# Kernel optimization log

Measured on AMD Instinct MI355X. Metric: run time of the kernel, lower is better.

The kernel has to match this reference:

```python
import jax, jax.numpy as jnp
import numpy as np

BATCH, SEQ, D_MODEL, K_SIZE = 2, 4096, 2048, 3


def setup_inputs() -> dict:
    key = jax.random.key(0)
    k1, k2, k3, k4 = jax.random.split(key, 4)
    s = 1.0 / np.sqrt(D_MODEL)
    x = jax.random.normal(k1, (BATCH, SEQ, D_MODEL), dtype=jnp.float32)
    w1 = jax.random.normal(k2, (3 * D_MODEL, D_MODEL), dtype=jnp.float32) * s
    w2 = jax.random.normal(k3, (D_MODEL, D_MODEL), dtype=jnp.float32) * s
    conv_w = jax.random.normal(k4, (D_MODEL, 1, K_SIZE), dtype=jnp.float32) * 0.5
    return {"x": x, "w1": w1, "w2": w2, "conv_w": conv_w}


def _causal_depthwise_conv(u, conv_w):
    # u: [B, D, S]; conv_w: [D, 1, K] (torch Conv1d weight layout, groups=D)
    k = conv_w.shape[-1]
    return jax.lax.conv_general_dilated(
        u, conv_w,
        window_strides=(1,),
        padding=[(k - 1, 0)],  # left pad = causal; matches pad=k-1 then [..., :seq_len]
        feature_group_count=u.shape[1],
        dimension_numbers=("NCH", "OIH", "NCH"),
    )


def reference(x, w1, w2, conv_w):
    # x: [B, S, D]
    BCx = jnp.einsum("bsd,ed->bse", x, w1)           # [B, S, 3D]
    Bg, Cg, Xg = jnp.split(BCx, 3, axis=-1)           # each [B, S, D]
    u = (Bg * Xg).transpose(0, 2, 1)                  # [B, D, S]
    conv_out = _causal_depthwise_conv(u, conv_w)      # [B, D, S]
    gated = Cg * conv_out.transpose(0, 2, 1)          # [B, S, D]
    return jnp.einsum("bsd,ed->bse", gated, w2)       # [B, S, D]
```

## Files before the change

kernel.cpp:

```cpp
#include <hip/hip_runtime.h>
#include <stdint.h>

#define BATCH 2
#define SEQ   4096
#define DM    2048
#define MT    (BATCH*SEQ)
#define N1    (3*DM)
#define STRIP 16

typedef __attribute__((ext_vector_type(8))) __bf16 bf16x8;
typedef __attribute__((ext_vector_type(4))) float  f32x4;
typedef __attribute__((ext_vector_type(8))) unsigned short ushort8v;
typedef __attribute__((ext_vector_type(4))) unsigned short ushort4v;

__device__ inline unsigned short f2bf(float f) {
    uint32_t u = __float_as_uint(f);
    u += 0x7FFFu + ((u >> 16) & 1u);
    return (unsigned short)(u >> 16);
}
__device__ inline float bf2f(unsigned short h) {
    return __uint_as_float(((uint32_t)h) << 16);
}

__global__ void cvt_f32_bf16(const float* __restrict__ src,
                             unsigned short* __restrict__ dst, int n) {
    int i = (blockIdx.x * blockDim.x + threadIdx.x) * 4;
    const int stride = gridDim.x * blockDim.x * 4;
    for (; i < n; i += stride) {
        const float4 v = *(const float4*)(src + i);
        ushort4v o;
        o[0] = f2bf(v.x); o[1] = f2bf(v.y); o[2] = f2bf(v.z); o[3] = f2bf(v.w);
        *(ushort4v*)(dst + i) = o;
    }
}

__device__ inline void async_copy16(const void* g, void* l) {
    __builtin_amdgcn_global_load_lds(
        (const __attribute__((address_space(1))) void*)g,
        (__attribute__((address_space(3))) void*)l,
        16, 0, 0);
}


#define MFMA_(d, a, b) d = __builtin_amdgcn_mfma_f32_16x16x32_bf16(a, b, d, 0, 0, 0)

#define QUAD(MH, NH, BQ) do { \
  MFMA_(acc[(MH)*4+0][(NH)*2+0], af[0][0], BQ[0][0]); MFMA_(acc[(MH)*4+0][(NH)*2+0], af[0][1], BQ[0][1]); \
  MFMA_(acc[(MH)*4+0][(NH)*2+1], af[0][0], BQ[1][0]); MFMA_(acc[(MH)*4+0][(NH)*2+1], af[0][1], BQ[1][1]); \
  MFMA_(acc[(MH)*4+1][(NH)*2+0], af[1][0], BQ[0][0]); MFMA_(acc[(MH)*4+1][(NH)*2+0], af[1][1], BQ[0][1]); \
  MFMA_(acc[(MH)*4+1][(NH)*2+1], af[1][0], BQ[1][0]); MFMA_(acc[(MH)*4+1][(NH)*2+1], af[1][1], BQ[1][1]); \
  MFMA_(acc[(MH)*4+2][(NH)*2+0], af[2][0], BQ[0][0]); MFMA_(acc[(MH)*4+2][(NH)*2+0], af[2][1], BQ[0][1]); \
  MFMA_(acc[(MH)*4+2][(NH)*2+1], af[2][0], BQ[1][0]); MFMA_(acc[(MH)*4+2][(NH)*2+1], af[2][1], BQ[1][1]); \
  MFMA_(acc[(MH)*4+3][(NH)*2+0], af[3][0], BQ[0][0]); MFMA_(acc[(MH)*4+3][(NH)*2+0], af[3][1], BQ[0][1]); \
  MFMA_(acc[(MH)*4+3][(NH)*2+1], af[3][0], BQ[1][0]); MFMA_(acc[(MH)*4+3][(NH)*2+1], af[3][1], BQ[1][1]); \
} while (0)

template <bool OUT_BF16>
__global__ __launch_bounds__(512)
void gemm256(const unsigned short* __restrict__ A,
             const unsigned short* __restrict__ B,
             void* __restrict__ Cout, int M, int N, int K) {
    __shared__ __attribute__((aligned(16))) char lds[131072];
    const int tid  = threadIdx.x;
    const int wave = tid >> 6;
    const int lane = tid & 63;
    const int wr = wave >> 2, wc = wave & 3;
    const int l16 = lane & 15, lh = lane >> 4;
    const int NT = K >> 6;

    const int nx = gridDim.x;
    int flat = blockIdx.y * nx + blockIdx.x;
    const int cpx = (nx * gridDim.y) >> 3;
    flat = (flat & 7) * cpx + (flat >> 3);
    const int blockN = (flat % nx) << 8;
    const int blockM = (flat / nx) << 8;

    const int swze = ((((lane & 7) << 4) ^ ((lane >> 3) << 4)) >> 1);
    const int sr   = (wave << 3) + (lane >> 3);
    const unsigned short* Ab = A + (size_t)blockM * K;
    const unsigned short* Bb = B + (size_t)blockN * K;
    const size_t a00 = (size_t)(sr      ) * K + swze;
    const size_t a01 = (size_t)(sr +  64) * K + swze;
    const size_t a10 = (size_t)(sr + 128) * K + swze;
    const size_t a11 = (size_t)(sr + 192) * K + swze;
    const int bsr = ((wave >> 2) << 6) + ((wave & 3) << 3) + (lane >> 3);
    const size_t b00 = (size_t)(bsr      ) * K + swze;
    const size_t b01 = (size_t)(bsr + 128) * K + swze;
    const size_t b10 = (size_t)(bsr +  32) * K + swze;
    const size_t b11 = (size_t)(bsr + 160) * K + swze;
    const int ldsw = wave << 10;

#define STG_A(BUF, U, K0) do { \
    async_copy16(Ab + a##U##0 + (K0), lds + (BUF) + (U)*16384 + ldsw); \
    async_copy16(Ab + a##U##1 + (K0), lds + (BUF) + (U)*16384 + 8192 + ldsw); } while (0)
#define STG_B(BUF, NH, K0) do { \
    async_copy16(Bb + b##NH##0 + (K0), lds + (BUF) + 32768 + (NH)*16384 + ldsw); \
    async_copy16(Bb + b##NH##1 + (K0), lds + (BUF) + 32768 + (NH)*16384 + 8192 + ldsw); } while (0)

    const int rdswz = (l16 & 7) << 4;
    const int ac0 = ((lh << 4)      ) ^ rdswz;
    const int ac1 = (64 + (lh << 4)) ^ rdswz;
    const int aRB = wr * 16384 + l16 * 128;
    const int bRB = 32768 + (wc * 32 + l16) * 128;

#define LDA_(BUF, I, C) (*(const bf16x8*)(lds + (BUF) + aRB + (I)*2048 + (C)))
#define LDB_(BUF, J, C) (*(const bf16x8*)(lds + (BUF) + bRB + ((J)>>1)*16384 + ((J)&1)*2048 + (C)))

    f32x4 acc[8][4] = {};
    bf16x8 af[4][2], bq0[2][2], bq1[2][2];

    STG_B(0, 0, 0); STG_B(0, 1, 0); STG_A(0, 0, 0); STG_A(0, 1, 0);
    if (NT > 1) {
        STG_B(65536, 0, 64); STG_B(65536, 1, 64); STG_A(65536, 0, 64);
        asm volatile("s_waitcnt vmcnt(6)" ::: "memory");
    } else {
        asm volatile("s_waitcnt vmcnt(0)" ::: "memory");
    }
    __builtin_amdgcn_s_barrier();

#define ITER(CUR, NXT, T) do { \
     \
    af[0][0]=LDA_(CUR,0,ac0); af[0][1]=LDA_(CUR,0,ac1); \
    af[1][0]=LDA_(CUR,1,ac0); af[1][1]=LDA_(CUR,1,ac1); \
    af[2][0]=LDA_(CUR,2,ac0); af[2][1]=LDA_(CUR,2,ac1); \
    af[3][0]=LDA_(CUR,3,ac0); af[3][1]=LDA_(CUR,3,ac1); \
    bq0[0][0]=LDB_(CUR,0,ac0); bq0[0][1]=LDB_(CUR,0,ac1); \
    bq0[1][0]=LDB_(CUR,1,ac0); bq0[1][1]=LDB_(CUR,1,ac1); \
    if ((T) + 1 < NT) STG_A(NXT, 1, ((T)+1)*64); \
    __builtin_amdgcn_s_barrier(); \
    asm volatile("s_waitcnt lgkmcnt(0)" ::: "memory"); \
    __builtin_amdgcn_s_setprio(1); \
    QUAD(0, 0, bq0); \
    __builtin_amdgcn_s_setprio(0); \
    __builtin_amdgcn_s_barrier(); \
     \
    bq1[0][0]=LDB_(CUR,2,ac0); bq1[0][1]=LDB_(CUR,2,ac1); \
    bq1[1][0]=LDB_(CUR,3,ac0); bq1[1][1]=LDB_(CUR,3,ac1); \
    if ((T) + 2 < NT) STG_B(CUR, 0, ((T)+2)*64); \
    __builtin_amdgcn_s_barrier(); \
    asm volatile("s_waitcnt lgkmcnt(0)" ::: "memory"); \
    __builtin_amdgcn_s_setprio(1); \
    QUAD(0, 1, bq1); \
    __builtin_amdgcn_s_setprio(0); \
    __builtin_amdgcn_s_barrier(); \
     \
    af[0][0]=LDA_(CUR,4,ac0); af[0][1]=LDA_(CUR,4,ac1); \
    af[1][0]=LDA_(CUR,5,ac0); af[1][1]=LDA_(CUR,5,ac1); \
    af[2][0]=LDA_(CUR,6,ac0); af[2][1]=LDA_(CUR,6,ac1); \
    af[3][0]=LDA_(CUR,7,ac0); af[3][1]=LDA_(CUR,7,ac1); \
    if ((T) + 2 < NT) STG_B(CUR, 1, ((T)+2)*64); \
    __builtin_amdgcn_s_barrier(); \
    asm volatile("s_waitcnt lgkmcnt(0)" ::: "memory"); \
    __builtin_amdgcn_s_setprio(1); \
    QUAD(1, 1, bq1); \
    __builtin_amdgcn_s_setprio(0); \
    __builtin_amdgcn_s_barrier(); \
     \
    if ((T) + 2 < NT) STG_A(CUR, 0, ((T)+2)*64); \
    __builtin_amdgcn_s_barrier(); \
    __builtin_amdgcn_s_setprio(1); \
    QUAD(1, 0, bq0); \
    __builtin_amdgcn_s_setprio(0); \
    if ((T) + 2 < NT)      { asm volatile("s_waitcnt vmcnt(6)" ::: "memory"); } \
    else if ((T) + 1 < NT) { asm volatile("s_waitcnt vmcnt(0)" ::: "memory"); } \
    __builtin_amdgcn_s_barrier(); \
} while (0)

    for (int t = 0; t < NT; t += 2) {
        ITER(0, 65536, t);
        ITER(65536, 0, t + 1);
    }

    const int orow = blockM + wr * 128 + (lh << 2);
    const int ocol = blockN + wc * 64 + l16;
    #pragma unroll
    for (int i = 0; i < 8; ++i) {
        #pragma unroll
        for (int j = 0; j < 4; ++j) {
            #pragma unroll
            for (int r = 0; r < 4; ++r) {
                const int row = orow + i * 16 + r;
                const int col = ocol + j * 16;
                if constexpr (OUT_BF16)
                    ((unsigned short*)Cout)[(size_t)row * N + col] = f2bf(acc[i][j][r]);
                else
                    ((float*)Cout)[(size_t)row * N + col] = acc[i][j][r];
            }
        }
    }
#undef ITER
#undef LDA_
#undef LDB_
#undef STG_A
#undef STG_B
}

__global__ void conv_gate_kernel(const unsigned short* __restrict__ BCx,
                                 const float* __restrict__ cw,
                                 unsigned short* __restrict__ gated) {
    const int tid = threadIdx.x;
    const int d0  = tid * 8;
    const int nstrips = SEQ / STRIP;
    const int b   = blockIdx.x / nstrips;
    const int s0  = (blockIdx.x % nstrips) * STRIP;

    float w0[8], w1c[8], w2c[8];
    #pragma unroll
    for (int c = 0; c < 8; ++c) {
        w0[c]  = cw[(d0 + c) * 3 + 0];
        w1c[c] = cw[(d0 + c) * 3 + 1];
        w2c[c] = cw[(d0 + c) * 3 + 2];
    }

    float um1[8], um2[8];
    if (s0 > 0) {
        const unsigned short* r2 = BCx + (size_t)(b * SEQ + s0 - 2) * N1;
        const unsigned short* r1 = BCx + (size_t)(b * SEQ + s0 - 1) * N1;
        ushort8v bg2 = *(const ushort8v*)(r2 + d0);
        ushort8v xg2 = *(const ushort8v*)(r2 + 2 * DM + d0);
        ushort8v bg1 = *(const ushort8v*)(r1 + d0);
        ushort8v xg1 = *(const ushort8v*)(r1 + 2 * DM + d0);
        #pragma unroll
        for (int c = 0; c < 8; ++c) {
            um2[c] = bf2f(bg2[c]) * bf2f(xg2[c]);
            um1[c] = bf2f(bg1[c]) * bf2f(xg1[c]);
        }
    } else {
        #pragma unroll
        for (int c = 0; c < 8; ++c) { um2[c] = 0.f; um1[c] = 0.f; }
    }

    for (int s = s0; s < s0 + STRIP; ++s) {
        const size_t m = (size_t)b * SEQ + s;
        const unsigned short* rp = BCx + m * N1;
        ushort8v bg = *(const ushort8v*)(rp + d0);
        ushort8v cg = *(const ushort8v*)(rp + DM + d0);
        ushort8v xg = *(const ushort8v*)(rp + 2 * DM + d0);
        ushort8v og;
        #pragma unroll
        for (int c = 0; c < 8; ++c) {
            const float u    = bf2f(bg[c]) * bf2f(xg[c]);
            const float conv = w0[c] * um2[c] + w1c[c] * um1[c] + w2c[c] * u;
            const float g    = bf2f(cg[c]) * conv;
            um2[c] = um1[c];
            um1[c] = u;
            og[c]  = f2bf(g);
        }
        *(ushort8v*)(gated + m * DM + d0) = og;
    }
}

extern "C" void kernel_launch(void* const* d_in, const int* in_sizes, int n_in,
                              void* d_out, int out_size, void* d_ws, size_t ws_size,
                              hipStream_t stream) {
    const float* x   = (const float*)d_in[0];
    const float* w1  = (const float*)d_in[1];
    const float* w2  = (const float*)d_in[2];
    const float* cw  = (const float*)d_in[3];
    float* out = (float*)d_out;

    char* ws = (char*)d_ws;
    unsigned short* x_bf   = (unsigned short*)ws;
    unsigned short* w1_bf  = x_bf  + (size_t)MT * DM;
    unsigned short* w2_bf  = w1_bf + (size_t)N1 * DM;
    unsigned short* bcx_bf = w2_bf + (size_t)DM * DM;
    unsigned short* g_bf   = bcx_bf + (size_t)MT * N1;

    cvt_f32_bf16<<<2048, 256, 0, stream>>>(x,  x_bf,  MT * DM);
    cvt_f32_bf16<<<1024, 256, 0, stream>>>(w1, w1_bf, N1 * DM);
    cvt_f32_bf16<<<512,  256, 0, stream>>>(w2, w2_bf, DM * DM);

    gemm256<true><<<dim3(N1 / 256, MT / 256), 512, 0, stream>>>(
        x_bf, w1_bf, bcx_bf, MT, N1, DM);

    conv_gate_kernel<<<BATCH * (SEQ / STRIP), 256, 0, stream>>>(bcx_bf, cw, g_bf);

    gemm256<false><<<dim3(DM / 256, MT / 256), 512, 0, stream>>>(
        g_bf, w2_bf, out, MT, DM, DM);
}
```

Measured before the change: 311.7 us.

## Double-buffer A fragments and prefetch next tile's fragments across iterations

Splits the A register fragments into low and high halves so both stay live, reorders the four MFMA quadrants so each LDS read is issued one phase ahead with partial lgkmcnt waits, and preloads the next K-tile's first fragments at the end of each iteration. It also restructures the global-to-LDS staging schedule, prefetching the whole second tile up front and adjusting the vmcnt thresholds. The aim is to hide LDS read latency behind MFMA work and cut the full lgkmcnt(0) stalls, at the cost of more VGPRs and a more fragile barrier and waitcnt ordering.

```diff
diff --git a/kernel.cpp b/kernel.cpp
--- a/kernel.cpp
+++ b/kernel.cpp
@@ -44,15 +44,15 @@
 
 #define MFMA_(d, a, b) d = __builtin_amdgcn_mfma_f32_16x16x32_bf16(a, b, d, 0, 0, 0)
 
-#define QUAD(MH, NH, BQ) do { \
-  MFMA_(acc[(MH)*4+0][(NH)*2+0], af[0][0], BQ[0][0]); MFMA_(acc[(MH)*4+0][(NH)*2+0], af[0][1], BQ[0][1]); \
-  MFMA_(acc[(MH)*4+0][(NH)*2+1], af[0][0], BQ[1][0]); MFMA_(acc[(MH)*4+0][(NH)*2+1], af[0][1], BQ[1][1]); \
-  MFMA_(acc[(MH)*4+1][(NH)*2+0], af[1][0], BQ[0][0]); MFMA_(acc[(MH)*4+1][(NH)*2+0], af[1][1], BQ[0][1]); \
-  MFMA_(acc[(MH)*4+1][(NH)*2+1], af[1][0], BQ[1][0]); MFMA_(acc[(MH)*4+1][(NH)*2+1], af[1][1], BQ[1][1]); \
-  MFMA_(acc[(MH)*4+2][(NH)*2+0], af[2][0], BQ[0][0]); MFMA_(acc[(MH)*4+2][(NH)*2+0], af[2][1], BQ[0][1]); \
-  MFMA_(acc[(MH)*4+2][(NH)*2+1], af[2][0], BQ[1][0]); MFMA_(acc[(MH)*4+2][(NH)*2+1], af[2][1], BQ[1][1]); \
-  MFMA_(acc[(MH)*4+3][(NH)*2+0], af[3][0], BQ[0][0]); MFMA_(acc[(MH)*4+3][(NH)*2+0], af[3][1], BQ[0][1]); \
-  MFMA_(acc[(MH)*4+3][(NH)*2+1], af[3][0], BQ[1][0]); MFMA_(acc[(MH)*4+3][(NH)*2+1], af[3][1], BQ[1][1]); \
+#define QUAD(MH, NH, AF, BQ) do { \
+  MFMA_(acc[(MH)*4+0][(NH)*2+0], AF[0][0], BQ[0][0]); MFMA_(acc[(MH)*4+0][(NH)*2+0], AF[0][1], BQ[0][1]); \
+  MFMA_(acc[(MH)*4+0][(NH)*2+1], AF[0][0], BQ[1][0]); MFMA_(acc[(MH)*4+0][(NH)*2+1], AF[0][1], BQ[1][1]); \
+  MFMA_(acc[(MH)*4+1][(NH)*2+0], AF[1][0], BQ[0][0]); MFMA_(acc[(MH)*4+1][(NH)*2+0], AF[1][1], BQ[0][1]); \
+  MFMA_(acc[(MH)*4+1][(NH)*2+1], AF[1][0], BQ[1][0]); MFMA_(acc[(MH)*4+1][(NH)*2+1], AF[1][1], BQ[1][1]); \
+  MFMA_(acc[(MH)*4+2][(NH)*2+0], AF[2][0], BQ[0][0]); MFMA_(acc[(MH)*4+2][(NH)*2+0], AF[2][1], BQ[0][1]); \
+  MFMA_(acc[(MH)*4+2][(NH)*2+1], AF[2][0], BQ[1][0]); MFMA_(acc[(MH)*4+2][(NH)*2+1], AF[2][1], BQ[1][1]); \
+  MFMA_(acc[(MH)*4+3][(NH)*2+0], AF[3][0], BQ[0][0]); MFMA_(acc[(MH)*4+3][(NH)*2+0], AF[3][1], BQ[0][1]); \
+  MFMA_(acc[(MH)*4+3][(NH)*2+1], AF[3][0], BQ[1][0]); MFMA_(acc[(MH)*4+3][(NH)*2+1], AF[3][1], BQ[1][1]); \
 } while (0)
 
 template <bool OUT_BF16>
@@ -107,30 +107,34 @@
 #define LDB_(BUF, J, C) (*(const bf16x8*)(lds + (BUF) + bRB + ((J)>>1)*16384 + ((J)&1)*2048 + (C)))
 
     f32x4 acc[8][4] = {};
-    bf16x8 af[4][2], bq0[2][2], bq1[2][2];
+    bf16x8 afL[4][2], afH[4][2], bq0[2][2], bq1[2][2];
 
     STG_B(0, 0, 0); STG_B(0, 1, 0); STG_A(0, 0, 0); STG_A(0, 1, 0);
     if (NT > 1) {
-        STG_B(65536, 0, 64); STG_B(65536, 1, 64); STG_A(65536, 0, 64);
-        asm volatile("s_waitcnt vmcnt(6)" ::: "memory");
+        STG_B(65536, 0, 64); STG_B(65536, 1, 64);
+        STG_A(65536, 0, 64); STG_A(65536, 1, 64);
+        asm volatile("s_waitcnt vmcnt(8)" ::: "memory");
     } else {
         asm volatile("s_waitcnt vmcnt(0)" ::: "memory");
     }
     __builtin_amdgcn_s_barrier();
+    afL[0][0]=LDA_(0,0,ac0); afL[0][1]=LDA_(0,0,ac1);
+    afL[1][0]=LDA_(0,1,ac0); afL[1][1]=LDA_(0,1,ac1);
+    afL[2][0]=LDA_(0,2,ac0); afL[2][1]=LDA_(0,2,ac1);
+    afL[3][0]=LDA_(0,3,ac0); afL[3][1]=LDA_(0,3,ac1);
+    bq0[0][0]=LDB_(0,0,ac0); bq0[0][1]=LDB_(0,0,ac1);
+    bq0[1][0]=LDB_(0,1,ac0); bq0[1][1]=LDB_(0,1,ac1);
 
 #define ITER(CUR, NXT, T) do { \
      \
-    af[0][0]=LDA_(CUR,0,ac0); af[0][1]=LDA_(CUR,0,ac1); \
-    af[1][0]=LDA_(CUR,1,ac0); af[1][1]=LDA_(CUR,1,ac1); \
-    af[2][0]=LDA_(CUR,2,ac0); af[2][1]=LDA_(CUR,2,ac1); \
-    af[3][0]=LDA_(CUR,3,ac0); af[3][1]=LDA_(CUR,3,ac1); \
-    bq0[0][0]=LDB_(CUR,0,ac0); bq0[0][1]=LDB_(CUR,0,ac1); \
-    bq0[1][0]=LDB_(CUR,1,ac0); bq0[1][1]=LDB_(CUR,1,ac1); \
-    if ((T) + 1 < NT) STG_A(NXT, 1, ((T)+1)*64); \
-    __builtin_amdgcn_s_barrier(); \
-    asm volatile("s_waitcnt lgkmcnt(0)" ::: "memory"); \
-    __builtin_amdgcn_s_setprio(1); \
-    QUAD(0, 0, bq0); \
+    afH[0][0]=LDA_(CUR,4,ac0); afH[0][1]=LDA_(CUR,4,ac1); \
+    afH[1][0]=LDA_(CUR,5,ac0); afH[1][1]=LDA_(CUR,5,ac1); \
+    afH[2][0]=LDA_(CUR,6,ac0); afH[2][1]=LDA_(CUR,6,ac1); \
+    afH[3][0]=LDA_(CUR,7,ac0); afH[3][1]=LDA_(CUR,7,ac1); \
+    __builtin_amdgcn_s_barrier(); \
+    asm volatile("s_waitcnt lgkmcnt(8)" ::: "memory"); \
+    __builtin_amdgcn_s_setprio(1); \
+    QUAD(0, 0, afL, bq0); \
     __builtin_amdgcn_s_setprio(0); \
     __builtin_amdgcn_s_barrier(); \
      \
@@ -138,31 +142,33 @@
     bq1[1][0]=LDB_(CUR,3,ac0); bq1[1][1]=LDB_(CUR,3,ac1); \
     if ((T) + 2 < NT) STG_B(CUR, 0, ((T)+2)*64); \
     __builtin_amdgcn_s_barrier(); \
+    asm volatile("s_waitcnt lgkmcnt(4)" ::: "memory"); \
+    __builtin_amdgcn_s_setprio(1); \
+    QUAD(1, 0, afH, bq0); \
+    __builtin_amdgcn_s_setprio(0); \
+    __builtin_amdgcn_s_barrier(); \
+     \
+    if ((T) + 2 < NT) STG_A(CUR, 0, ((T)+2)*64); \
+    __builtin_amdgcn_s_barrier(); \
     asm volatile("s_waitcnt lgkmcnt(0)" ::: "memory"); \
     __builtin_amdgcn_s_setprio(1); \
-    QUAD(0, 1, bq1); \
-    __builtin_amdgcn_s_setprio(0); \
-    __builtin_amdgcn_s_barrier(); \
-     \
-    af[0][0]=LDA_(CUR,4,ac0); af[0][1]=LDA_(CUR,4,ac1); \
-    af[1][0]=LDA_(CUR,5,ac0); af[1][1]=LDA_(CUR,5,ac1); \
-    af[2][0]=LDA_(CUR,6,ac0); af[2][1]=LDA_(CUR,6,ac1); \
-    af[3][0]=LDA_(CUR,7,ac0); af[3][1]=LDA_(CUR,7,ac1); \
-    if ((T) + 2 < NT) STG_B(CUR, 1, ((T)+2)*64); \
-    __builtin_amdgcn_s_barrier(); \
-    asm volatile("s_waitcnt lgkmcnt(0)" ::: "memory"); \
-    __builtin_amdgcn_s_setprio(1); \
-    QUAD(1, 1, bq1); \
-    __builtin_amdgcn_s_setprio(0); \
-    __builtin_amdgcn_s_barrier(); \
-     \
-    if ((T) + 2 < NT) STG_A(CUR, 0, ((T)+2)*64); \
-    __builtin_amdgcn_s_barrier(); \
-    __builtin_amdgcn_s_setprio(1); \
-    QUAD(1, 0, bq0); \
-    __builtin_amdgcn_s_setprio(0); \
-    if ((T) + 2 < NT)      { asm volatile("s_waitcnt vmcnt(6)" ::: "memory"); } \
+    QUAD(0, 1, afL, bq1); \
+    __builtin_amdgcn_s_setprio(0); \
+    if ((T) + 2 < NT)      { asm volatile("s_waitcnt vmcnt(4)" ::: "memory"); } \
     else if ((T) + 1 < NT) { asm volatile("s_waitcnt vmcnt(0)" ::: "memory"); } \
+    __builtin_amdgcn_s_barrier(); \
+     \
+    afL[0][0]=LDA_(NXT,0,ac0); afL[0][1]=LDA_(NXT,0,ac1); \
+    afL[1][0]=LDA_(NXT,1,ac0); afL[1][1]=LDA_(NXT,1,ac1); \
+    afL[2][0]=LDA_(NXT,2,ac0); afL[2][1]=LDA_(NXT,2,ac1); \
+    afL[3][0]=LDA_(NXT,3,ac0); afL[3][1]=LDA_(NXT,3,ac1); \
+    bq0[0][0]=LDB_(NXT,0,ac0); bq0[0][1]=LDB_(NXT,0,ac1); \
+    bq0[1][0]=LDB_(NXT,1,ac0); bq0[1][1]=LDB_(NXT,1,ac1); \
+    if ((T) + 2 < NT) { STG_A(CUR, 1, ((T)+2)*64); STG_B(CUR, 1, ((T)+2)*64); } \
+    __builtin_amdgcn_s_barrier(); \
+    __builtin_amdgcn_s_setprio(1); \
+    QUAD(1, 1, afH, bq1); \
+    __builtin_amdgcn_s_setprio(0); \
     __builtin_amdgcn_s_barrier(); \
 } while (0)
 
```

Result: slower. 523.5 us (+68.0%).
